# Optimization experiments

Hardware: AMD Instinct MI355X
Metric: run time of the kernel (lower is better)

The kernel has to match this reference:

```python
import jax, jax.numpy as jnp
import numpy as np

HEAD_DIM = 128


def block_causal_mask(cu_seqlens, seq_len, dtype):
    # positions -> which packed document each token belongs to
    positions = jnp.arange(seq_len)
    seq_ids = jnp.searchsorted(cu_seqlens, positions, side='right') - 1
    same_seq = seq_ids[:, None] == seq_ids[None, :]
    causal = positions[None, :] <= positions[:, None]  # key_pos <= query_pos
    neg_inf = jnp.asarray(float('-inf'), dtype)
    return jnp.where(same_seq & causal, jnp.asarray(0.0, dtype), neg_inf)


def setup_inputs() -> dict:
    key = jax.random.key(0)
    kq, kk, kv = jax.random.split(key, 3)
    B, H, S, D = 1, 8, 4096, HEAD_DIM
    q = jax.random.normal(kq, (B, H, S, D), dtype=jnp.float32)
    k = jax.random.normal(kk, (B, H, S, D), dtype=jnp.float32)
    v = jax.random.normal(kv, (B, H, S, D), dtype=jnp.float32)
    # 4 packed documents of length 1024 each; cu_seqlens[-1] == seq_len
    cu_seqlens = jnp.array([0, 1024, 2048, 3072, 4096], dtype=jnp.int32)
    return {"q": q, "k": k, "v": v, "cu_seqlens": cu_seqlens, "max_seqlen": 1024}


def reference(q, k, v, cu_seqlens, max_seqlen):
    seq_len = q.shape[2]
    scale = 1.0 / jnp.sqrt(jnp.asarray(q.shape[-1], q.dtype))
    mask = block_causal_mask(cu_seqlens, seq_len, q.dtype)  # [S, S]
    # scores: [B, H, Sq, Sk]
    scores = jnp.einsum('bhqd,bhkd->bhqk', q, k) * scale + mask
    probs = jax.nn.softmax(scores, axis=-1)
    return jnp.einsum('bhqk,bhkd->bhqd', probs, v)
```

## Files before the change

kernel.cpp:

```cpp
#include <hip/hip_runtime.h>
#include <hip/hip_bf16.h>


#define HD 128
#define BR 64
#define BC 64
#define KSTR 136
#define VSTR 33
#define PSTR 68

typedef __attribute__((ext_vector_type(8))) short short8;
typedef __attribute__((ext_vector_type(4))) short short4v;
typedef __attribute__((ext_vector_type(4))) float floatx4;

__device__ inline unsigned short bfbits(float f) {
    __hip_bfloat16 b = __float2bfloat16(f);
    return *reinterpret_cast<unsigned short*>(&b);
}
__device__ inline short bfs(float f) {
    __hip_bfloat16 b = __float2bfloat16(f);
    return *reinterpret_cast<short*>(&b);
}

union F4 { float4 v; float f[4]; };

__global__ __launch_bounds__(256, 2) void fa_fwd(
    const float* __restrict__ Q,
    const float* __restrict__ K,
    const float* __restrict__ V,
    const int* __restrict__ cu_seqlens, int n_cu,
    float* __restrict__ O,
    int S)
{
    __shared__ alignas(16) __hip_bfloat16 sK[2][BC * KSTR];
    __shared__ alignas(16) unsigned int   sVT[2][HD * VSTR];
    __shared__ alignas(16) __hip_bfloat16 sP[4][16 * PSTR];

    const int tid  = threadIdx.x;
    const int wave = tid >> 6;
    const int lane = tid & 63;
    const int quad = lane >> 4;
    const int l16  = lane & 15;

    const int dblk = tid & 31;
    const int trow = tid >> 5;
    const int vd    = tid & 127;
    const int vhalf = tid >> 7;

    const int nqb = S / BR;
    const int h   = blockIdx.x & 7;
    const int qb  = nqb - 1 - (int)(blockIdx.x >> 3);
    const int q0  = qb * BR;
    const int qw  = q0 + wave * 16;

    const size_t hoff = (size_t)h * S * HD;
    const float* Qh = Q + hoff;
    const float* Kh = K + hoff;
    const float* Vh = V + hoff;
    float*       Oh = O + hoff;

    int doc_start[4];
    #pragma unroll
    for (int r = 0; r < 4; ++r) {
        const int q = qw + quad * 4 + r;
        int dsr = 0;
        for (int i = 0; i < n_cu; ++i) {
            int c = cu_seqlens[i];
            if (c <= q) dsr = c;
        }
        doc_start[r] = dsr;
    }
    int blk_ds = 0;
    for (int i = 0; i < n_cu; ++i) {
        int c = cu_seqlens[i];
        if (c <= q0) blk_ds = c;
    }
    const int k_begin = blk_ds & ~(BC - 1);
    const int ntiles  = (q0 + BR - 1 - k_begin) / BC + 1;

    short8 aq[4];
    {
        const float* qp = Qh + (size_t)(qw + l16) * HD + quad * 8;
        #pragma unroll
        for (int ks = 0; ks < 4; ++ks) {
            float4 a0 = *(const float4*)(qp + ks * 32);
            float4 a1 = *(const float4*)(qp + ks * 32 + 4);
            short8 a;
            a[0] = bfs(a0.x); a[1] = bfs(a0.y); a[2] = bfs(a0.z); a[3] = bfs(a0.w);
            a[4] = bfs(a1.x); a[5] = bfs(a1.y); a[6] = bfs(a1.z); a[7] = bfs(a1.w);
            aq[ks] = a;
        }
    }

    floatx4 oacc[8];
    #pragma unroll
    for (int dt = 0; dt < 8; ++dt) oacc[dt] = (floatx4){0.f, 0.f, 0.f, 0.f};
    float m_r[4], l_r[4];
    #pragma unroll
    for (int r = 0; r < 4; ++r) { m_r[r] = -1e30f; l_r[r] = 0.f; }

    const float sl = 0.08838834764831845f * 1.4426950408889634f;

    F4 kf[8];
    float vf[32];

    auto issue_loads = [&](int kt) {
        const float* kb = Kh + (size_t)kt * HD + 4 * dblk;
        #pragma unroll
        for (int p = 0; p < 8; ++p)
            kf[p].v = *(const float4*)(kb + (size_t)(trow + 8 * p) * HD);
        const float* vb = Vh + (size_t)(kt + vhalf * 32) * HD + vd;
        #pragma unroll
        for (int kk = 0; kk < 32; ++kk)
            vf[kk] = vb[(size_t)kk * HD];
    };

    auto write_tiles = [&](int buf) {
        #pragma unroll
        for (int p = 0; p < 8; ++p) {
            short4v hk;
            hk[0] = bfs(kf[p].f[0]); hk[1] = bfs(kf[p].f[1]);
            hk[2] = bfs(kf[p].f[2]); hk[3] = bfs(kf[p].f[3]);
            *(short4v*)(&sK[buf][(trow + 8 * p) * KSTR + 4 * dblk]) = hk;
        }
        unsigned* dst = &sVT[buf][vd * VSTR + vhalf * 16];
        #pragma unroll
        for (int kp = 0; kp < 16; ++kp)
            dst[kp] = ((unsigned)bfbits(vf[2 * kp + 1]) << 16) | bfbits(vf[2 * kp]);
    };

    issue_loads(k_begin);

    __hip_bfloat16* pbuf = &sP[wave][0];

    for (int it = 0; it < ntiles; ++it) {
        const int kt  = k_begin + it * BC;
        const int buf = it & 1;

        write_tiles(buf);
        __syncthreads();

        if (it + 1 < ntiles) issue_loads(kt + BC);

        floatx4 sc[4];
        #pragma unroll
        for (int ct = 0; ct < 4; ++ct) {
            if (kt + ct * 16 <= qw + 15) {
                floatx4 c = (floatx4){0.f, 0.f, 0.f, 0.f};
                #pragma unroll
                for (int ks = 0; ks < 4; ++ks) {
                    short8 b = *(const short8*)(&sK[buf][(ct * 16 + l16) * KSTR + ks * 32 + quad * 8]);
                    c = __builtin_amdgcn_mfma_f32_16x16x32_bf16(aq[ks], b, c, 0, 0, 0);
                }
                const int key = kt + ct * 16 + l16;
                #pragma unroll
                for (int r = 0; r < 4; ++r) {
                    const int q = qw + quad * 4 + r;
                    const bool valid = (key <= q) && (key >= doc_start[r]);
                    float s = c[r] * sl;
                    c[r] = valid ? s : -1e30f;
                }
                sc[ct] = c;
            } else {
                sc[ct] = (floatx4){-1e30f, -1e30f, -1e30f, -1e30f};
            }
        }

        float mx[4];
        #pragma unroll
        for (int r = 0; r < 4; ++r)
            mx[r] = fmaxf(fmaxf(sc[0][r], sc[1][r]), fmaxf(sc[2][r], sc[3][r]));
        #pragma unroll
        for (int off = 1; off < 16; off <<= 1) {
            #pragma unroll
            for (int r = 0; r < 4; ++r)
                mx[r] = fmaxf(mx[r], __shfl_xor(mx[r], off, 64));
        }
        float al[4];
        #pragma unroll
        for (int r = 0; r < 4; ++r) {
            const float mnew = fmaxf(m_r[r], mx[r]);
            al[r] = exp2f(m_r[r] - mnew);
            m_r[r] = mnew;
        }
        #pragma unroll
        for (int r = 0; r < 4; ++r) {
            float s0 = exp2f(sc[0][r] - m_r[r]);
            float s1 = exp2f(sc[1][r] - m_r[r]);
            float s2 = exp2f(sc[2][r] - m_r[r]);
            float s3 = exp2f(sc[3][r] - m_r[r]);
            sc[0][r] = s0; sc[1][r] = s1; sc[2][r] = s2; sc[3][r] = s3;
            l_r[r] = l_r[r] * al[r] + ((s0 + s1) + (s2 + s3));
        }
        #pragma unroll
        for (int dt = 0; dt < 8; ++dt) {
            #pragma unroll
            for (int r = 0; r < 4; ++r)
                oacc[dt][r] *= al[r];
        }

        #pragma unroll
        for (int ct = 0; ct < 4; ++ct)
            #pragma unroll
            for (int r = 0; r < 4; ++r)
                pbuf[(quad * 4 + r) * PSTR + ct * 16 + l16] = __float2bfloat16(sc[ct][r]);

        #pragma unroll
        for (int ks = 0; ks < 2; ++ks) {
            if (kt + ks * 32 <= qw + 15) {
                short4v lo = *(const short4v*)(&pbuf[l16 * PSTR + ks * 32 + quad * 8]);
                short4v hi = *(const short4v*)(&pbuf[l16 * PSTR + ks * 32 + quad * 8 + 4]);
                short8 ap = __builtin_shufflevector(lo, hi, 0, 1, 2, 3, 4, 5, 6, 7);
                #pragma unroll
                for (int dt = 0; dt < 8; ++dt) {
                    const unsigned* vp = &sVT[buf][(dt * 16 + l16) * VSTR + ks * 16 + quad * 4];
                    union { unsigned u[4]; short8 s; } cv;
                    cv.u[0] = vp[0]; cv.u[1] = vp[1]; cv.u[2] = vp[2]; cv.u[3] = vp[3];
                    oacc[dt] = __builtin_amdgcn_mfma_f32_16x16x32_bf16(ap, cv.s, oacc[dt], 0, 0, 0);
                }
            }
        }
    }

    #pragma unroll
    for (int off = 1; off < 16; off <<= 1) {
        #pragma unroll
        for (int r = 0; r < 4; ++r)
            l_r[r] += __shfl_xor(l_r[r], off, 64);
    }
    #pragma unroll
    for (int r = 0; r < 4; ++r) {
        const float inv = 1.0f / l_r[r];
        float* op = Oh + (size_t)(qw + quad * 4 + r) * HD;
        #pragma unroll
        for (int dt = 0; dt < 8; ++dt)
            op[dt * 16 + l16] = oacc[dt][r] * inv;
    }
}

extern "C" void kernel_launch(void* const* d_in, const int* in_sizes, int n_in,
                              void* d_out, int out_size, void* d_ws, size_t ws_size,
                              hipStream_t stream) {
    const float* q = (const float*)d_in[0];
    const float* k = (const float*)d_in[1];
    const float* v = (const float*)d_in[2];
    const int* cu = (const int*)d_in[3];
    const int n_cu = in_sizes[3];
    const int H = 8;
    const int S = in_sizes[0] / (H * HD);
    float* out = (float*)d_out;

    dim3 grid(H * (S / BR));
    dim3 block(256);
    fa_fwd<<<grid, block, 0, stream>>>(q, k, v, cu, n_cu, out, S);
}
```

Before: 141.6 us.

## Single-buffer LDS tiles for higher occupancy, reorder q-blocks, pack bf16 pairs

Replaces the double-buffered K/V shared tiles with single buffers and adds a trailing barrier per iteration, which cuts LDS use so the launch bound can be raised to three blocks per CU. Block-to-query-tile mapping is reordered for the 64-tile case so heavy and light causal blocks are interleaved across the grid for better load balance. bf16 conversion now uses paired float2-to-bfloat162 packing to reduce conversion instructions. The cost is an extra __syncthreads per tile and tighter register pressure at the higher occupancy target.

```diff
diff --git a/kernel.cpp b/kernel.cpp
--- a/kernel.cpp
+++ b/kernel.cpp
@@ -13,9 +13,9 @@
 typedef __attribute__((ext_vector_type(4))) short short4v;
 typedef __attribute__((ext_vector_type(4))) float floatx4;
 
-__device__ inline unsigned short bfbits(float f) {
-    __hip_bfloat16 b = __float2bfloat16(f);
-    return *reinterpret_cast<unsigned short*>(&b);
+__device__ inline unsigned packbf2(float lo, float hi) {
+    __hip_bfloat162 h2 = __float22bfloat162_rn(make_float2(lo, hi));
+    return *reinterpret_cast<unsigned*>(&h2);
 }
 __device__ inline short bfs(float f) {
     __hip_bfloat16 b = __float2bfloat16(f);
@@ -24,7 +24,7 @@
 
 union F4 { float4 v; float f[4]; };
 
-__global__ __launch_bounds__(256, 2) void fa_fwd(
+__global__ __launch_bounds__(256, 3) void fa_fwd(
     const float* __restrict__ Q,
     const float* __restrict__ K,
     const float* __restrict__ V,
@@ -32,8 +32,8 @@
     float* __restrict__ O,
     int S)
 {
-    __shared__ alignas(16) __hip_bfloat16 sK[2][BC * KSTR];
-    __shared__ alignas(16) unsigned int   sVT[2][HD * VSTR];
+    __shared__ alignas(16) __hip_bfloat16 sK[BC * KSTR];
+    __shared__ alignas(16) unsigned int   sVT[HD * VSTR];
     __shared__ alignas(16) __hip_bfloat16 sP[4][16 * PSTR];
 
     const int tid  = threadIdx.x;
@@ -49,7 +49,14 @@
 
     const int nqb = S / BR;
     const int h   = blockIdx.x & 7;
-    const int qb  = nqb - 1 - (int)(blockIdx.x >> 3);
+    const int g   = (int)(blockIdx.x >> 3);
+    int qb;
+    if (nqb == 64) {
+        if (g < 32) qb = (g >> 4) * 16 + (15 - (g & 15));
+        else        qb = 32 + (((g - 32) >> 4) * 16) + (g & 15);
+    } else {
+        qb = nqb - 1 - g;
+    }
     const int q0  = qb * BR;
     const int qw  = q0 + wave * 16;
 
@@ -115,18 +122,18 @@
             vf[kk] = vb[(size_t)kk * HD];
     };
 
-    auto write_tiles = [&](int buf) {
+    auto write_tiles = [&]() {
         #pragma unroll
         for (int p = 0; p < 8; ++p) {
-            short4v hk;
-            hk[0] = bfs(kf[p].f[0]); hk[1] = bfs(kf[p].f[1]);
-            hk[2] = bfs(kf[p].f[2]); hk[3] = bfs(kf[p].f[3]);
-            *(short4v*)(&sK[buf][(trow + 8 * p) * KSTR + 4 * dblk]) = hk;
-        }
-        unsigned* dst = &sVT[buf][vd * VSTR + vhalf * 16];
+            uint2 kw;
+            kw.x = packbf2(kf[p].f[0], kf[p].f[1]);
+            kw.y = packbf2(kf[p].f[2], kf[p].f[3]);
+            *(uint2*)(&sK[(trow + 8 * p) * KSTR + 4 * dblk]) = kw;
+        }
+        unsigned* dst = &sVT[vd * VSTR + vhalf * 16];
         #pragma unroll
         for (int kp = 0; kp < 16; ++kp)
-            dst[kp] = ((unsigned)bfbits(vf[2 * kp + 1]) << 16) | bfbits(vf[2 * kp]);
+            dst[kp] = packbf2(vf[2 * kp], vf[2 * kp + 1]);
     };
 
     issue_loads(k_begin);
@@ -134,10 +141,9 @@
     __hip_bfloat16* pbuf = &sP[wave][0];
 
     for (int it = 0; it < ntiles; ++it) {
-        const int kt  = k_begin + it * BC;
-        const int buf = it & 1;
-
-        write_tiles(buf);
+        const int kt = k_begin + it * BC;
+
+        write_tiles();
         __syncthreads();
 
         if (it + 1 < ntiles) issue_loads(kt + BC);
@@ -149,7 +155,7 @@
                 floatx4 c = (floatx4){0.f, 0.f, 0.f, 0.f};
                 #pragma unroll
                 for (int ks = 0; ks < 4; ++ks) {
-                    short8 b = *(const short8*)(&sK[buf][(ct * 16 + l16) * KSTR + ks * 32 + quad * 8]);
+                    short8 b = *(const short8*)(&sK[(ct * 16 + l16) * KSTR + ks * 32 + quad * 8]);
                     c = __builtin_amdgcn_mfma_f32_16x16x32_bf16(aq[ks], b, c, 0, 0, 0);
                 }
                 const int key = kt + ct * 16 + l16;
@@ -213,13 +219,15 @@
                 short8 ap = __builtin_shufflevector(lo, hi, 0, 1, 2, 3, 4, 5, 6, 7);
                 #pragma unroll
                 for (int dt = 0; dt < 8; ++dt) {
-                    const unsigned* vp = &sVT[buf][(dt * 16 + l16) * VSTR + ks * 16 + quad * 4];
+                    const unsigned* vp = &sVT[(dt * 16 + l16) * VSTR + ks * 16 + quad * 4];
                     union { unsigned u[4]; short8 s; } cv;
                     cv.u[0] = vp[0]; cv.u[1] = vp[1]; cv.u[2] = vp[2]; cv.u[3] = vp[3];
                     oacc[dt] = __builtin_amdgcn_mfma_f32_16x16x32_bf16(ap, cv.s, oacc[dt], 0, 0, 0);
                 }
             }
         }
+
+        __syncthreads();
     }
 
     #pragma unroll
```

Measured after the change: 174.6 us. 1.23x slower.
